# Optimization experiments

Measured on AMD Instinct MI355X. Metric: run time of the kernel, lower is better.

## Reference

```python
import jax, jax.numpy as jnp
import numpy as np

N, E = 50000, 800000
NODE_DIM, EDGE_DIM, HEADS = 64, 16, 4
C = NODE_DIM // HEADS  # per-head channels
NEG_SLOPE = 0.2
BN_EPS = 1e-5


def setup_inputs() -> dict:
    key = jax.random.key(0)
    ks = jax.random.split(key, 12)
    glorot = lambda k, shape: jax.random.normal(k, shape, jnp.float32) * np.sqrt(2.0 / (shape[0] + shape[-1]))
    return {
        "x": jax.random.normal(ks[0], (N, NODE_DIM), jnp.float32),
        "edge_index": jax.random.randint(ks[1], (2, E), 0, N, jnp.int32),
        "edge_attr": jax.random.normal(ks[2], (E, EDGE_DIM), jnp.float32),
        "W_l": glorot(ks[3], (NODE_DIM, HEADS * C)),
        "b_l": jnp.zeros((HEADS * C,), jnp.float32),
        "W_r": glorot(ks[4], (NODE_DIM, HEADS * C)),
        "b_r": jnp.zeros((HEADS * C,), jnp.float32),
        "W_e": glorot(ks[5], (EDGE_DIM, HEADS * C)),
        "att": glorot(ks[6], (HEADS, C)),
        "bias": jnp.zeros((HEADS * C,), jnp.float32),
        "gamma": jnp.ones((NODE_DIM,), jnp.float32),
        "beta": jnp.zeros((NODE_DIM,), jnp.float32),
    }


def reference(x, edge_index, edge_attr, W_l, b_l, W_r, b_r, W_e, att, bias, gamma, beta):
    src, dst = edge_index[0], edge_index[1]
    n = x.shape[0]
    # GATv2: node transforms for source (l) and target (r) roles
    xl = (x @ W_l + b_l).reshape(n, HEADS, C)
    xr = (x @ W_r + b_r).reshape(n, HEADS, C)
    e = (edge_attr @ W_e).reshape(-1, HEADS, C)
    # per-edge attention logits: leaky_relu(x_j + x_i + e) . att  -> [E, H]
    g = jax.nn.leaky_relu(xl[src] + xr[dst] + e, NEG_SLOPE)
    logits = jnp.einsum('ehc,hc->eh', g, att)
    # segment softmax grouped by destination node
    amax = jax.ops.segment_max(logits, dst, num_segments=n)
    ex = jnp.exp(logits - amax[dst])
    denom = jax.ops.segment_sum(ex, dst, num_segments=n)
    alpha = ex / (denom[dst] + 1e-16)  # [E, H]
    # weighted message aggregation (scatter-add over dst), concat heads
    msg = xl[src] * alpha[..., None]  # [E, H, C]
    out = jax.ops.segment_sum(msg, dst, num_segments=n).reshape(n, HEADS * C) + bias
    # BatchNorm (training-mode batch statistics over nodes)
    mean = out.mean(axis=0)
    var = out.var(axis=0)
    out = (out - mean) * jax.lax.rsqrt(var + BN_EPS) * gamma + beta
    # residual + exact GELU
    return jax.nn.gelu(out + x, approximate=False)
```

## Files before the change

### kernel.cpp

```cpp
#include <hip/hip_runtime.h>
#include <hip/hip_fp16.h>
#include <math.h>

#define NODE_DIM 64
#define EDGE_DIM 16
#define CAP 64
#define NEG_SLOPE 0.2f
#define BN_EPS 1e-5f

typedef unsigned short ushort_t;
typedef unsigned int uint_t;
typedef __fp16 h2_t __attribute__((ext_vector_type(2)));

template<int CTRL>
__device__ __forceinline__ float dpp_mov_f(float v) {
    return __int_as_float(__builtin_amdgcn_update_dpp(
        0, __float_as_int(v), CTRL, 0xF, 0xF, true));
}
__device__ __forceinline__ float row_sum16(float v) {
    v += dpp_mov_f<0x128>(v);
    v += dpp_mov_f<0x124>(v);
    v += dpp_mov_f<0x122>(v);
    v += dpp_mov_f<0x121>(v);
    return v;
}
__device__ __forceinline__ float wave_sum64(float v) {
    v = row_sum16(v);
    v += __shfl_xor(v, 16, 64);
    v += __shfl_xor(v, 32, 64);
    return v;
}
__device__ __forceinline__ float wave_max64(float v) {
    v = fmaxf(v, dpp_mov_f<0x128>(v));
    v = fmaxf(v, dpp_mov_f<0x124>(v));
    v = fmaxf(v, dpp_mov_f<0x122>(v));
    v = fmaxf(v, dpp_mov_f<0x121>(v));
    v = fmaxf(v, __shfl_xor(v, 16, 64));
    v = fmaxf(v, __shfl_xor(v, 32, 64));
    return v;
}
__device__ __forceinline__ ushort_t f2bf(float f) {
    unsigned int b = __float_as_uint(f);
    b += 0x7FFFu + ((b >> 16) & 1u);
    return (ushort_t)(b >> 16);
}
__device__ __forceinline__ float bf2f(ushort_t u) {
    return __uint_as_float(((unsigned int)u) << 16);
}
__device__ __forceinline__ uint_t packh2(float a, float b) {
    __half2 h;
    h.x = __float2half_rn(a);
    h.y = __float2half_rn(b);
    return *reinterpret_cast<uint_t*>(&h);
}
__device__ __forceinline__ float2 unpackh2(uint_t u) {
    __half2 h = *reinterpret_cast<__half2*>(&u);
    return make_float2(__half2float(h.x), __half2float(h.y));
}
__device__ __forceinline__ float fdot2u(uint_t a, uint_t b, float c) {
#if __has_builtin(__builtin_amdgcn_fdot2)
    union { uint_t u; h2_t h; } ua, ub;
    ua.u = a; ub.u = b;
    return __builtin_amdgcn_fdot2(ua.h, ub.h, c, false);
#else
    float2 fa = unpackh2(a), fb = unpackh2(b);
    return fmaf(fa.y, fb.y, fmaf(fa.x, fb.x, c));
#endif
}

__global__ __launch_bounds__(256) void k_transform(
    const float* __restrict__ x, const float* __restrict__ Wl,
    const float* __restrict__ bl, const float* __restrict__ Wr,
    const float* __restrict__ br, ushort_t* __restrict__ xlbf,
    ushort_t* __restrict__ xrbf, int n)
{
    int lane = threadIdx.x & 63;
    int wid = threadIdx.x >> 6;

    uint_t wlp[32], wrp[32];
#pragma unroll
    for (int m = 0; m < 32; m++) {
        wlp[m] = packh2(Wl[(2 * m) * NODE_DIM + lane],
                        Wl[(2 * m + 1) * NODE_DIM + lane]);
        wrp[m] = packh2(Wr[(2 * m) * NODE_DIM + lane],
                        Wr[(2 * m + 1) * NODE_DIM + lane]);
    }
    float blc = bl[lane], brc = br[lane];

    for (int row = blockIdx.x * 4 + wid; row < n; row += gridDim.x * 4) {
        const float4* x4 = (const float4*)(x + (size_t)row * NODE_DIM);
        float al = blc, ar = brc;
#pragma unroll
        for (int p = 0; p < 16; p++) {
            float4 v = x4[p];
            uint_t x01 = packh2(v.x, v.y);
            uint_t x23 = packh2(v.z, v.w);
            al = fdot2u(x01, wlp[2 * p], al);
            al = fdot2u(x23, wlp[2 * p + 1], al);
            ar = fdot2u(x01, wrp[2 * p], ar);
            ar = fdot2u(x23, wrp[2 * p + 1], ar);
        }
        xlbf[(size_t)row * NODE_DIM + lane] = f2bf(al);
        xrbf[(size_t)row * NODE_DIM + lane] = f2bf(ar);
    }
}

__global__ __launch_bounds__(256) void k_edge(
    const int* __restrict__ ei, const float* __restrict__ eattr,
    const float* __restrict__ We, const float* __restrict__ att,
    int* __restrict__ cursors,
    const ushort_t* __restrict__ xlbf, const ushort_t* __restrict__ xrbf,
    uint4* __restrict__ payload, int E)
{
    __shared__ uint_t sea[4][64 * 8];
    __shared__ float slg[4][64 * 4];

    int lane = threadIdx.x & 63;
    int wid = threadIdx.x >> 6;
    int wbase = (blockIdx.x * 4 + wid) * 64;
    if (wbase >= E) return;
    wbase = __builtin_amdgcn_readfirstlane(wbase);
    int cnt = E - wbase; if (cnt > 64) cnt = 64;

    {
        const float4* esrc = (const float4*)(eattr + (size_t)wbase * EDGE_DIM);
        uint2* sdst = (uint2*)sea[wid];
        int lim = cnt * 4;
#pragma unroll
        for (int r = 0; r < 4; r++) {
            int idx = r * 64 + lane;
            if (idx < lim) {
                float4 v = esrc[idx];
                sdst[idx] = make_uint2(packh2(v.x, v.y), packh2(v.z, v.w));
            }
        }
    }

    uint_t wep[8];
#pragma unroll
    for (int m = 0; m < 8; m++)
        wep[m] = packh2(We[(2 * m) * NODE_DIM + lane],
                        We[(2 * m + 1) * NODE_DIM + lane]);
    float att_p = att[lane];
    float att_n = att_p * NEG_SLOPE;

    int src_l = 0, pos_l = CAP, dst_l = 0;
    if (lane < cnt) {
        src_l = ei[wbase + lane];
        dst_l = ei[E + wbase + lane];
        pos_l = atomicAdd(&cursors[dst_l], 1);
    }
    int dst_l_bc = dst_l;

    uint_t* seaW = sea[wid];

    ushort_t pxl[8], pxr[8];
    auto LOADT = [&](int t, int k) {
        int s = __builtin_amdgcn_readlane(src_l, t);
        int d = __builtin_amdgcn_readlane(dst_l_bc, t);
        pxl[k] = xlbf[(size_t)s * NODE_DIM + lane];
        pxr[k] = xrbf[(size_t)d * NODE_DIM + lane];
    };
    auto LOGIT = [&](int t, int k) -> float {
        const uint4* e4 = (const uint4*)(seaW + t * 8);
        uint4 ea0 = e4[0], ea1 = e4[1];
        float p0 = 0.f, p1 = 0.f;
        p0 = fdot2u(ea0.x, wep[0], p0);  p1 = fdot2u(ea0.y, wep[1], p1);
        p0 = fdot2u(ea0.z, wep[2], p0);  p1 = fdot2u(ea0.w, wep[3], p1);
        p0 = fdot2u(ea1.x, wep[4], p0);  p1 = fdot2u(ea1.y, wep[5], p1);
        p0 = fdot2u(ea1.z, wep[6], p0);  p1 = fdot2u(ea1.w, wep[7], p1);
        float sv = bf2f(pxl[k]) + bf2f(pxr[k]) + (p0 + p1);
        float g = sv * (sv > 0.f ? att_p : att_n);
        return row_sum16(g);
    };

    if (cnt == 64) {
        float kp[4];
#pragma unroll
        for (int k = 0; k < 8; k++) LOADT(k, k);
#pragma unroll
        for (int t = 0; t < 64; t++) {
            float g = LOGIT(t, t & 7);
            if ((lane & 15) == (t & 15)) kp[t >> 4] = g;
            if (t + 8 < 64) LOADT(t + 8, (t + 8) & 7);
        }
        int h4 = lane >> 4;
        float xA = (h4 & 1) ? kp[0] : kp[1];
        float yA = (h4 & 1) ? kp[2] : kp[3];
        xA = __shfl_xor(xA, 16, 64);
        yA = __shfl_xor(yA, 16, 64);
        float A0 = (h4 & 1) ? xA : kp[0];
        float A1 = (h4 & 1) ? kp[1] : xA;
        float A2 = (h4 & 1) ? yA : kp[2];
        float A3 = (h4 & 1) ? kp[3] : yA;
        float xB = (h4 & 2) ? A0 : A2;
        float yB = (h4 & 2) ? A1 : A3;
        xB = __shfl_xor(xB, 32, 64);
        yB = __shfl_xor(yB, 32, 64);
        float B0 = (h4 & 2) ? xB : A0;
        float B1 = (h4 & 2) ? yB : A1;
        float B2 = (h4 & 2) ? A2 : xB;
        float B3 = (h4 & 2) ? A3 : yB;
        if (pos_l < CAP)
            payload[(size_t)dst_l * CAP + pos_l] =
                make_uint4((uint_t)src_l, packh2(B0, B1), packh2(B2, B3), 0u);
    } else {
        float* slgW = slg[wid];
        for (int t = 0; t < cnt; t++) {
            int s = __builtin_amdgcn_readlane(src_l, t);
            int d = __builtin_amdgcn_readlane(dst_l_bc, t);
            pxl[0] = xlbf[(size_t)s * NODE_DIM + lane];
            pxr[0] = xrbf[(size_t)d * NODE_DIM + lane];
            float g = LOGIT(t, 0);
            if ((lane & 15) == 0) slgW[t * 4 + (lane >> 4)] = g;
        }
        __builtin_amdgcn_s_waitcnt(0);
        if (lane < cnt && pos_l < CAP) {
            float4 lg4 = ((const float4*)slgW)[lane];
            payload[(size_t)dst_l * CAP + pos_l] =
                make_uint4((uint_t)src_l, packh2(lg4.x, lg4.y),
                           packh2(lg4.z, lg4.w), 0u);
        }
    }
}

__global__ __launch_bounds__(256) void k_fused(
    const uint4* __restrict__ payload, const int* __restrict__ cursors,
    const ushort_t* __restrict__ xlbf, const float* __restrict__ bias,
    float* __restrict__ out, int n)
{
    __shared__ float salpha[4][CAP * 4];
    __shared__ int ssrc[4][CAP];

    int wid = threadIdx.x >> 6;
    int lane = threadIdx.x & 63;
    int i = blockIdx.x * 4 + wid;
    if (i >= n) return;

    int deg = cursors[i];
    if (deg > CAP) deg = CAP;
    bool act = (lane < deg);

    uint4 pl = act ? payload[(size_t)i * CAP + lane] : make_uint4(0u, 0u, 0u, 0u);
    int se_x = (int)pl.x;
    float2 g01 = unpackh2(pl.y);
    float2 g23 = unpackh2(pl.z);

    float l0 = act ? g01.x : -1e30f;
    float l1 = act ? g01.y : -1e30f;
    float l2 = act ? g23.x : -1e30f;
    float l3 = act ? g23.y : -1e30f;
    float m0 = wave_max64(l0), m1 = wave_max64(l1);
    float m2 = wave_max64(l2), m3 = wave_max64(l3);
    float e0 = act ? __expf(l0 - m0) : 0.f;
    float e1 = act ? __expf(l1 - m1) : 0.f;
    float e2 = act ? __expf(l2 - m2) : 0.f;
    float e3 = act ? __expf(l3 - m3) : 0.f;
    float s0 = wave_sum64(e0), s1 = wave_sum64(e1);
    float s2 = wave_sum64(e2), s3 = wave_sum64(e3);
    float* salW = salpha[wid];
    int* ssrcW = ssrc[wid];
    ((float4*)salW)[lane] = make_float4(
        e0 / (s0 + 1e-16f), e1 / (s1 + 1e-16f),
        e2 / (s2 + 1e-16f), e3 / (s3 + 1e-16f));
    ssrcW[lane] = se_x;

    int r = lane >> 3, c = lane & 7;
    float a0 = 0.f, a1 = 0.f, a2 = 0.f, a3 = 0.f;
    float a4 = 0.f, a5 = 0.f, a6 = 0.f, a7 = 0.f;
    int nb = (deg + 7) >> 3;

    uint4 v0, v1, v2, v3, v4, v5, v6, v7;
#define LDV(B, V)                                                        \
    if ((B) < nb) {                                                      \
        int st = ssrcW[(B) * 8 + r];                                     \
        V = *(const uint4*)(xlbf + (size_t)st * NODE_DIM + c * 8);       \
    }
    LDV(0, v0) LDV(1, v1) LDV(2, v2) LDV(3, v3)
    LDV(4, v4) LDV(5, v5) LDV(6, v6) LDV(7, v7)
#undef LDV

#define ACC(B, V)                                                        \
    if ((B) < nb) {                                                      \
        float al = salW[((B) * 8 + r) * 4 + (c >> 1)];                   \
        a0 = fmaf(al, __uint_as_float(V.x << 16), a0);                   \
        a1 = fmaf(al, __uint_as_float(V.x & 0xFFFF0000u), a1);           \
        a2 = fmaf(al, __uint_as_float(V.y << 16), a2);                   \
        a3 = fmaf(al, __uint_as_float(V.y & 0xFFFF0000u), a3);           \
        a4 = fmaf(al, __uint_as_float(V.z << 16), a4);                   \
        a5 = fmaf(al, __uint_as_float(V.z & 0xFFFF0000u), a5);           \
        a6 = fmaf(al, __uint_as_float(V.w << 16), a6);                   \
        a7 = fmaf(al, __uint_as_float(V.w & 0xFFFF0000u), a7);           \
    }
    ACC(0, v0) ACC(1, v1) ACC(2, v2) ACC(3, v3)
    ACC(4, v4) ACC(5, v5) ACC(6, v6) ACC(7, v7)
#undef ACC

#define RED(x) do { \
        x += dpp_mov_f<0x128>(x); \
        x += __shfl_xor(x, 16, 64); \
        x += __shfl_xor(x, 32, 64); } while (0)
    RED(a0); RED(a1); RED(a2); RED(a3);
    RED(a4); RED(a5); RED(a6); RED(a7);
#undef RED
    float t0 = (r & 1) ? a1 : a0;
    float t1 = (r & 1) ? a3 : a2;
    float t2 = (r & 1) ? a5 : a4;
    float t3 = (r & 1) ? a7 : a6;
    float u0 = (r & 2) ? t1 : t0;
    float u1 = (r & 2) ? t3 : t2;
    float w  = (r & 4) ? u1 : u0;
    int ch = c * 8 + r;
    out[(size_t)i * NODE_DIM + ch] = w + bias[ch];
}

__global__ __launch_bounds__(256) void k_bnstat(
    const float* __restrict__ out, float* __restrict__ stats, int n)
{
    __shared__ float sbuf[256];
    int col = threadIdx.x & 63;
    int rgrp = threadIdx.x >> 6;
    float s = 0.f, q = 0.f;
    for (int row = blockIdx.x * 4 + rgrp; row < n; row += gridDim.x * 4) {
        float v = out[(size_t)row * 64 + col];
        s += v;
        q = fmaf(v, v, q);
    }
    sbuf[threadIdx.x] = s;
    __syncthreads();
    if (threadIdx.x < 64) {
        s = sbuf[threadIdx.x] + sbuf[threadIdx.x + 64] +
            sbuf[threadIdx.x + 128] + sbuf[threadIdx.x + 192];
        atomicAdd(&stats[col], s);
    }
    __syncthreads();
    sbuf[threadIdx.x] = q;
    __syncthreads();
    if (threadIdx.x < 64) {
        q = sbuf[threadIdx.x] + sbuf[threadIdx.x + 64] +
            sbuf[threadIdx.x + 128] + sbuf[threadIdx.x + 192];
        atomicAdd(&stats[64 + col], q);
    }
}

__global__ __launch_bounds__(256) void k_final(
    float* __restrict__ out, const float* __restrict__ x,
    const float* __restrict__ stats, const float* __restrict__ gamma,
    const float* __restrict__ beta, int total, float invn)
{
    int i = blockIdx.x * 256 + threadIdx.x;
    if (i >= total) return;
    int c = i & 63;
    float mean = stats[c] * invn;
    float var = stats[64 + c] * invn - mean * mean;
    float z = (out[i] - mean) * rsqrtf(var + BN_EPS) * gamma[c] + beta[c] + x[i];
    out[i] = z * 0.5f * (1.f + erff(z * 0.70710678118654752f));
}

extern "C" void kernel_launch(void* const* d_in, const int* in_sizes, int n_in,
                              void* d_out, int out_size, void* d_ws, size_t ws_size,
                              hipStream_t stream)
{
    const float* x     = (const float*)d_in[0];
    const int*   ei    = (const int*)d_in[1];
    const float* eattr = (const float*)d_in[2];
    const float* Wl    = (const float*)d_in[3];
    const float* bl    = (const float*)d_in[4];
    const float* Wr    = (const float*)d_in[5];
    const float* br    = (const float*)d_in[6];
    const float* We    = (const float*)d_in[7];
    const float* att   = (const float*)d_in[8];
    const float* bias  = (const float*)d_in[9];
    const float* gamma = (const float*)d_in[10];
    const float* beta  = (const float*)d_in[11];
    int n = in_sizes[0] / NODE_DIM;
    int E = in_sizes[1] / 2;

    char* ws = (char*)d_ws;
    ushort_t* xlbf    = (ushort_t*)ws; ws += (size_t)n * NODE_DIM * 2;
    ushort_t* xrbf    = (ushort_t*)ws; ws += (size_t)n * NODE_DIM * 2;
    uint4*    payload = (uint4*)ws;    ws += (size_t)n * CAP * 16;
    int*      cursors = (int*)ws;      ws += (size_t)n * 4;
    float*    stats   = (float*)ws;    ws += 128 * 4;

    hipMemsetAsync(cursors, 0, (size_t)(n + 128) * 4, stream);

    k_transform<<<1024, 256, 0, stream>>>(x, Wl, bl, Wr, br, xlbf, xrbf, n);
    k_edge<<<(E + 255) / 256, 256, 0, stream>>>(
        ei, eattr, We, att, cursors, xlbf, xrbf, payload, E);
    k_fused<<<(n + 3) / 4, 256, 0, stream>>>(
        payload, cursors, xlbf, bias, (float*)d_out, n);
    k_bnstat<<<256, 256, 0, stream>>>((const float*)d_out, stats, n);
    k_final<<<(n * NODE_DIM + 255) / 256, 256, 0, stream>>>(
        (float*)d_out, x, stats, gamma, beta, n * NODE_DIM, 1.0f / n);
}
```

Before: 165.4 us.

## Replace fixed-capacity per-node payload buckets with CSR offsets from count and scan

Adds a degree-count kernel and a single-block prefix scan, so the edge payload is stored compactly in CSR order (E entries) instead of n*CAP padded slots. This shrinks the payload footprint and makes each node's reads contiguous. The aggregation kernel also now issues the gathers of neighbor features before the softmax reductions so the two overlap. The cost is two extra launches, including a serial single-block scan over 50k nodes. Nodes with degree above CAP still have only their first CAP edges aggregated.

```diff
diff --git a/kernel.cpp b/kernel.cpp
--- a/kernel.cpp
+++ b/kernel.cpp
@@ -105,10 +105,40 @@
     }
 }
 
+__global__ __launch_bounds__(256) void k_count(
+    const int* __restrict__ ei, int* __restrict__ counts, int E)
+{
+    int e = blockIdx.x * 256 + threadIdx.x;
+    if (e >= E) return;
+    atomicAdd(&counts[ei[E + e]], 1);
+}
+
+__global__ __launch_bounds__(256) void k_scan(
+    const int* __restrict__ counts, int* __restrict__ offs, int n)
+{
+    __shared__ int ssum[256];
+    int tid = threadIdx.x;
+    int chunk = (n + 255) / 256;
+    int lo = tid * chunk;
+    int hi = lo + chunk; if (hi > n) hi = n;
+    int s = 0;
+    for (int j = lo; j < hi; j++) s += counts[j];
+    ssum[tid] = s;
+    __syncthreads();
+    for (int d = 1; d < 256; d <<= 1) {
+        int v = (tid >= d) ? ssum[tid - d] : 0;
+        __syncthreads();
+        ssum[tid] += v;
+        __syncthreads();
+    }
+    int base = (tid == 0) ? 0 : ssum[tid - 1];
+    for (int j = lo; j < hi; j++) { offs[j] = base; base += counts[j]; }
+}
+
 __global__ __launch_bounds__(256) void k_edge(
     const int* __restrict__ ei, const float* __restrict__ eattr,
     const float* __restrict__ We, const float* __restrict__ att,
-    int* __restrict__ cursors,
+    const int* __restrict__ offs, int* __restrict__ cursors,
     const ushort_t* __restrict__ xlbf, const ushort_t* __restrict__ xrbf,
     uint4* __restrict__ payload, int E)
 {
@@ -144,11 +174,11 @@
     float att_p = att[lane];
     float att_n = att_p * NEG_SLOPE;
 
-    int src_l = 0, pos_l = CAP, dst_l = 0;
+    int src_l = 0, pos_l = 0, dst_l = 0;
     if (lane < cnt) {
         src_l = ei[wbase + lane];
         dst_l = ei[E + wbase + lane];
-        pos_l = atomicAdd(&cursors[dst_l], 1);
+        pos_l = offs[dst_l] + atomicAdd(&cursors[dst_l], 1);
     }
     int dst_l_bc = dst_l;
 
@@ -201,9 +231,8 @@
         float B1 = (h4 & 2) ? yB : A1;
         float B2 = (h4 & 2) ? A2 : xB;
         float B3 = (h4 & 2) ? A3 : yB;
-        if (pos_l < CAP)
-            payload[(size_t)dst_l * CAP + pos_l] =
-                make_uint4((uint_t)src_l, packh2(B0, B1), packh2(B2, B3), 0u);
+        payload[pos_l] =
+            make_uint4((uint_t)src_l, packh2(B0, B1), packh2(B2, B3), 0u);
     } else {
         float* slgW = slg[wid];
         for (int t = 0; t < cnt; t++) {
@@ -215,9 +244,9 @@
             if ((lane & 15) == 0) slgW[t * 4 + (lane >> 4)] = g;
         }
         __builtin_amdgcn_s_waitcnt(0);
-        if (lane < cnt && pos_l < CAP) {
+        if (lane < cnt) {
             float4 lg4 = ((const float4*)slgW)[lane];
-            payload[(size_t)dst_l * CAP + pos_l] =
+            payload[pos_l] =
                 make_uint4((uint_t)src_l, packh2(lg4.x, lg4.y),
                            packh2(lg4.z, lg4.w), 0u);
         }
@@ -225,9 +254,9 @@
 }
 
 __global__ __launch_bounds__(256) void k_fused(
-    const uint4* __restrict__ payload, const int* __restrict__ cursors,
-    const ushort_t* __restrict__ xlbf, const float* __restrict__ bias,
-    float* __restrict__ out, int n)
+    const uint4* __restrict__ payload, const int* __restrict__ offs,
+    const int* __restrict__ counts, const ushort_t* __restrict__ xlbf,
+    const float* __restrict__ bias, float* __restrict__ out, int n)
 {
     __shared__ float salpha[4][CAP * 4];
     __shared__ int ssrc[4][CAP];
@@ -237,14 +266,32 @@
     int i = blockIdx.x * 4 + wid;
     if (i >= n) return;
 
-    int deg = cursors[i];
+    int deg = counts[i];
     if (deg > CAP) deg = CAP;
+    int base = offs[i];
     bool act = (lane < deg);
 
-    uint4 pl = act ? payload[(size_t)i * CAP + lane] : make_uint4(0u, 0u, 0u, 0u);
+    uint4 pl = act ? payload[(size_t)base + lane] : make_uint4(0u, 0u, 0u, 0u);
     int se_x = (int)pl.x;
     float2 g01 = unpackh2(pl.y);
     float2 g23 = unpackh2(pl.z);
+
+    float* salW = salpha[wid];
+    int* ssrcW = ssrc[wid];
+
+    ssrcW[lane] = se_x;
+    int r = lane >> 3, c = lane & 7;
+    int nb = (deg + 7) >> 3;
+
+    uint4 v0, v1, v2, v3, v4, v5, v6, v7;
+#define LDV(B, V)                                                        \
+    if ((B) < nb) {                                                      \
+        int st = ssrcW[(B) * 8 + r];                                     \
+        V = *(const uint4*)(xlbf + (size_t)st * NODE_DIM + c * 8);       \
+    }
+    LDV(0, v0) LDV(1, v1) LDV(2, v2) LDV(3, v3)
+    LDV(4, v4) LDV(5, v5) LDV(6, v6) LDV(7, v7)
+#undef LDV
 
     float l0 = act ? g01.x : -1e30f;
     float l1 = act ? g01.y : -1e30f;
@@ -258,28 +305,12 @@
     float e3 = act ? __expf(l3 - m3) : 0.f;
     float s0 = wave_sum64(e0), s1 = wave_sum64(e1);
     float s2 = wave_sum64(e2), s3 = wave_sum64(e3);
-    float* salW = salpha[wid];
-    int* ssrcW = ssrc[wid];
     ((float4*)salW)[lane] = make_float4(
         e0 / (s0 + 1e-16f), e1 / (s1 + 1e-16f),
         e2 / (s2 + 1e-16f), e3 / (s3 + 1e-16f));
-    ssrcW[lane] = se_x;
-
-    int r = lane >> 3, c = lane & 7;
+
     float a0 = 0.f, a1 = 0.f, a2 = 0.f, a3 = 0.f;
     float a4 = 0.f, a5 = 0.f, a6 = 0.f, a7 = 0.f;
-    int nb = (deg + 7) >> 3;
-
-    uint4 v0, v1, v2, v3, v4, v5, v6, v7;
-#define LDV(B, V)                                                        \
-    if ((B) < nb) {                                                      \
-        int st = ssrcW[(B) * 8 + r];                                     \
-        V = *(const uint4*)(xlbf + (size_t)st * NODE_DIM + c * 8);       \
-    }
-    LDV(0, v0) LDV(1, v1) LDV(2, v2) LDV(3, v3)
-    LDV(4, v4) LDV(5, v5) LDV(6, v6) LDV(7, v7)
-#undef LDV
-
 #define ACC(B, V)                                                        \
     if ((B) < nb) {                                                      \
         float al = salW[((B) * 8 + r) * 4 + (c >> 1)];                   \
@@ -379,17 +410,21 @@
     char* ws = (char*)d_ws;
     ushort_t* xlbf    = (ushort_t*)ws; ws += (size_t)n * NODE_DIM * 2;
     ushort_t* xrbf    = (ushort_t*)ws; ws += (size_t)n * NODE_DIM * 2;
-    uint4*    payload = (uint4*)ws;    ws += (size_t)n * CAP * 16;
+    uint4*    payload = (uint4*)ws;    ws += (size_t)E * 16;
+    int*      offs    = (int*)ws;      ws += (size_t)n * 4;
+    int*      counts  = (int*)ws;      ws += (size_t)n * 4;
     int*      cursors = (int*)ws;      ws += (size_t)n * 4;
     float*    stats   = (float*)ws;    ws += 128 * 4;
 
-    hipMemsetAsync(cursors, 0, (size_t)(n + 128) * 4, stream);
+    hipMemsetAsync(counts, 0, (size_t)(2 * n + 128) * 4, stream);
 
     k_transform<<<1024, 256, 0, stream>>>(x, Wl, bl, Wr, br, xlbf, xrbf, n);
+    k_count<<<(E + 255) / 256, 256, 0, stream>>>(ei, counts, E);
+    k_scan<<<1, 256, 0, stream>>>(counts, offs, n);
     k_edge<<<(E + 255) / 256, 256, 0, stream>>>(
-        ei, eattr, We, att, cursors, xlbf, xrbf, payload, E);
+        ei, eattr, We, att, offs, cursors, xlbf, xrbf, payload, E);
     k_fused<<<(n + 3) / 4, 256, 0, stream>>>(
-        payload, cursors, xlbf, bias, (float*)d_out, n);
+        payload, offs, counts, xlbf, bias, (float*)d_out, n);
     k_bnstat<<<256, 256, 0, stream>>>((const float*)d_out, stats, n);
     k_final<<<(n * NODE_DIM + 255) / 256, 256, 0, stream>>>(
         (float*)d_out, x, stats, gamma, beta, n * NODE_DIM, 1.0f / n);
```

After: 286.4 us. +73.1%, slower.
